# Optimization experiments

Hardware: AMD Instinct MI355X
Metric: run time of the kernel (lower is better)

Reference implementation:

```python
import jax, jax.numpy as jnp
import numpy as np

S, B, H = 256, 64, 1024


def setup_inputs() -> dict:
    key = jax.random.key(0)
    ks = jax.random.split(key, 8)
    scale = 1.0 / np.sqrt(2 * H)  # nn.Linear default-ish scale
    return {
        "x": jax.random.normal(ks[0], (S, B, H), dtype=jnp.float32),
        "h0": jax.random.normal(ks[1], (B, H), dtype=jnp.float32),
        "c0": jax.random.normal(ks[2], (B, H), dtype=jnp.float32),
        "Wf": jax.random.normal(ks[3], (H, 2 * H), dtype=jnp.float32) * scale,
        "bf": jnp.zeros((H,), dtype=jnp.float32),
        "Wi": jax.random.normal(ks[4], (H, 2 * H), dtype=jnp.float32) * scale,
        "bi": jnp.zeros((H,), dtype=jnp.float32),
        "Wg": jax.random.normal(ks[5], (H, 2 * H), dtype=jnp.float32) * scale,
        "bg": jnp.zeros((H,), dtype=jnp.float32),
        "Wo": jax.random.normal(ks[6], (H, 2 * H), dtype=jnp.float32) * scale,
        "bo": jnp.zeros((H,), dtype=jnp.float32),
    }


def _lstm(x, h0, c0, Wf, bf, Wi, bi, Wg, bg, Wo, bo):
    nhid = h0.shape[-1]
    # Fuse the 4 gate Linears into one GEMM: W_all [4H, 2H], b_all [4H].
    W_all = jnp.concatenate([Wf, Wi, Wg, Wo], axis=0)
    b_all = jnp.concatenate([bf, bi, bg, bo], axis=0)
    Wx, Wh = W_all[:, :nhid], W_all[:, nhid:]  # x-part / h-part of cat([x,h])
    # Precompute input contribution for all timesteps: [S, B, 4H]
    xz = jnp.einsum("sbh,gh->sbg", x, Wx) + b_all

    def step(carry, xz_t):
        h, c = carry
        z = xz_t + h @ Wh.T  # [B, 4H]
        f, i, g, o = jnp.split(z, 4, axis=-1)
        f = jax.nn.sigmoid(f)
        i = jax.nn.sigmoid(i)
        g = jnp.tanh(g)
        o = jax.nn.sigmoid(o)
        c = f * c + i * g
        h = o * jnp.tanh(c)
        return (h, c), h

    (h_f, c_f), hseq = jax.lax.scan(step, (h0, c0), xz)
    return hseq, h_f, c_f


def reference(x, h0, c0, Wf, bf, Wi, bi, Wg, bg, Wo, bo):
    hseq, h_f, c_f = _lstm(x, h0, c0, Wf, bf, Wi, bi, Wg, bg, Wo, bo)
    # residual_con=False path in the original: return x + hidden_seq
    return x + hseq, h_f, c_f
```

## Files before the change

kernel.cpp:

```cpp
#include <hip/hip_runtime.h>

typedef __bf16 bf16x8 __attribute__((ext_vector_type(8)));
typedef float f32x4 __attribute__((ext_vector_type(4)));
typedef unsigned int u32x4 __attribute__((ext_vector_type(4)));

#define S_LEN 256
#define BATCH 64
#define HID   1024
#define NWG   256
#define SBH   (S_LEN * BATCH * HID)
#define BH    (BATCH * HID)

__device__ __forceinline__ float sigm(float v) { return 1.0f / (1.0f + __expf(-v)); }
__device__ __forceinline__ float tanh_fast(float v) {
  float e = __expf(-2.0f * __builtin_fabsf(v));
  float r = (1.0f - e) / (1.0f + e);
  return __builtin_copysignf(r, v);
}

__device__ __forceinline__ u32x4 cvt8(float4 a, float4 b) {
  union { unsigned short us[8]; u32x4 v; } r;
  r.us[0] = __builtin_bit_cast(unsigned short, (__bf16)a.x);
  r.us[1] = __builtin_bit_cast(unsigned short, (__bf16)a.y);
  r.us[2] = __builtin_bit_cast(unsigned short, (__bf16)a.z);
  r.us[3] = __builtin_bit_cast(unsigned short, (__bf16)a.w);
  r.us[4] = __builtin_bit_cast(unsigned short, (__bf16)b.x);
  r.us[5] = __builtin_bit_cast(unsigned short, (__bf16)b.y);
  r.us[6] = __builtin_bit_cast(unsigned short, (__bf16)b.z);
  r.us[7] = __builtin_bit_cast(unsigned short, (__bf16)b.w);
  return r.v;
}

#define LOAD8_X4(dst, base, MODS)                                             \
  asm volatile(                                                               \
      "global_load_dwordx4 %0, %8, off offset:0 " MODS "\n\t"                 \
      "global_load_dwordx4 %1, %8, off offset:64 " MODS "\n\t"                \
      "global_load_dwordx4 %2, %8, off offset:128 " MODS "\n\t"               \
      "global_load_dwordx4 %3, %8, off offset:192 " MODS "\n\t"               \
      "global_load_dwordx4 %4, %8, off offset:256 " MODS "\n\t"               \
      "global_load_dwordx4 %5, %8, off offset:320 " MODS "\n\t"               \
      "global_load_dwordx4 %6, %8, off offset:384 " MODS "\n\t"               \
      "global_load_dwordx4 %7, %8, off offset:448 " MODS "\n\t"               \
      "s_waitcnt vmcnt(0)"                                                    \
      : "=&v"((dst)[0]), "=&v"((dst)[1]), "=&v"((dst)[2]), "=&v"((dst)[3]),   \
        "=&v"((dst)[4]), "=&v"((dst)[5]), "=&v"((dst)[6]), "=&v"((dst)[7])    \
      : "v"(base)                                                             \
      : "memory")

__global__ void prep_kernel(const float* __restrict__ x, const float* __restrict__ h0,
                            const float* __restrict__ Wf, const float* __restrict__ Wi,
                            const float* __restrict__ Wg, const float* __restrict__ Wo,
                            __bf16* __restrict__ x_bf, __bf16* __restrict__ w_x,
                            __bf16* __restrict__ w_h, __bf16* __restrict__ h_buf) {
  size_t tid = (size_t)blockIdx.x * blockDim.x + threadIdx.x;
  size_t stride = (size_t)gridDim.x * blockDim.x;

  for (size_t i = tid; i < (size_t)(SBH / 8); i += stride) {
    const float4* s = (const float4*)x + i * 2;
    ((u32x4*)x_bf)[i] = cvt8(s[0], s[1]);
  }

#define W_CONV(W, gidx)                                                        \
  for (size_t i = tid; i < (size_t)(1024 * 128); i += stride) {                \
    int j   = (int)(i >> 7);                                                   \
    int kc8 = (int)(i & 127);                                                  \
    const float* row = (W) + (size_t)j * 2048;                                 \
    const float4* sx = (const float4*)(row + kc8 * 8);                         \
    const float4* sh = (const float4*)(row + 1024 + kc8 * 8);                  \
    size_t dst = (size_t)((gidx) * 1024 + j) * 128 + kc8;                      \
    ((u32x4*)w_x)[dst] = cvt8(sx[0], sx[1]);                                   \
    ((u32x4*)w_h)[dst] = cvt8(sh[0], sh[1]);                                   \
  }
  W_CONV(Wf, 0)
  W_CONV(Wi, 1)
  W_CONV(Wg, 2)
  W_CONV(Wo, 3)
#undef W_CONV

  for (size_t i = tid; i < (size_t)(BH / 8); i += stride) {
    const float4* s = (const float4*)h0 + i * 2;
    u32x4 v = cvt8(s[0], s[1]);
    v &= 0xFFFEFFFEu;
    ((u32x4*)h_buf)[i] = v;
  }

  for (size_t i = tid; i < (size_t)(BH / 8); i += stride) {
    u32x4 p = {0x00010001u, 0x00010001u, 0x00010001u, 0x00010001u};
    ((u32x4*)(h_buf + BH))[i] = p;
  }
}

__global__ __launch_bounds__(256, 1) void lstm_kernel(
    const float* __restrict__ x, const float* __restrict__ c0,
    const float* __restrict__ bfp, const float* __restrict__ bip,
    const float* __restrict__ bgp, const float* __restrict__ bop,
    const __bf16* __restrict__ x_bf, const __bf16* __restrict__ w_x,
    const __bf16* __restrict__ w_h, __bf16* __restrict__ h_buf,
    float* __restrict__ out) {
  const int tid    = threadIdx.x;
  const int wgid   = blockIdx.x;
  const int m_idx  = wgid & 3;
  const int m_base = m_idx * 16;
  const int U      = (wgid >> 2) * 16;
  const int wave   = tid >> 6;
  const int lane   = tid & 63;
  const int l16    = lane & 15;
  const int kq8    = (lane >> 4) * 8;
  const int kbase  = wave * 256;

  __shared__ float zbuf[2][4][16][65];
  __shared__ unsigned short hpack[16][16];

  u32x4 Braw[64];
#pragma unroll
  for (int n = 0; n < 4; ++n) {
    unsigned long gbh =
        (unsigned long)(w_h + (size_t)(n * 1024 + U + l16) * HID + kbase + kq8);
    LOAD8_X4(&Braw[n * 8], gbh, "");
  }
#pragma unroll
  for (int n = 0; n < 4; ++n) {
    unsigned long gbx =
        (unsigned long)(w_x + (size_t)(n * 1024 + U + l16) * HID + kbase + kq8);
    LOAD8_X4(&Braw[32 + n * 8], gbx, "");
  }

  const int b_loc  = tid >> 4;
  const int u_loc  = tid & 15;
  const int j_t    = U + u_loc;
  const int b_glob = m_base + b_loc;
  float c = c0[(size_t)b_glob * HID + j_t];
  const float bias_f = bfp[j_t], bias_i = bip[j_t], bias_g = bgp[j_t], bias_o = bop[j_t];

  u32x4 Araw_x[8];
  {
    const __bf16* xp = x_bf + (size_t)(m_base + l16) * HID + kbase + kq8;
#pragma unroll
    for (int kc = 0; kc < 8; ++kc) Araw_x[kc] = *(const u32x4*)(xp + kc * 32);
  }
  f32x4 accx0 = {0,0,0,0}, accx1 = {0,0,0,0}, accx2 = {0,0,0,0}, accx3 = {0,0,0,0};
#pragma unroll
  for (int kc = 0; kc < 8; ++kc) {
    bf16x8 a = __builtin_bit_cast(bf16x8, Araw_x[kc]);
    accx0 = __builtin_amdgcn_mfma_f32_16x16x32_bf16(a, __builtin_bit_cast(bf16x8, Braw[32 +  0 + kc]), accx0, 0, 0, 0);
    accx1 = __builtin_amdgcn_mfma_f32_16x16x32_bf16(a, __builtin_bit_cast(bf16x8, Braw[32 +  8 + kc]), accx1, 0, 0, 0);
    accx2 = __builtin_amdgcn_mfma_f32_16x16x32_bf16(a, __builtin_bit_cast(bf16x8, Braw[32 + 16 + kc]), accx2, 0, 0, 0);
    accx3 = __builtin_amdgcn_mfma_f32_16x16x32_bf16(a, __builtin_bit_cast(bf16x8, Braw[32 + 24 + kc]), accx3, 0, 0, 0);
  }
  {
    const __bf16* xp = x_bf + (size_t)(BATCH + m_base + l16) * HID + kbase + kq8;
#pragma unroll
    for (int kc = 0; kc < 8; ++kc) Araw_x[kc] = *(const u32x4*)(xp + kc * 32);
  }

  for (int t = 0; t < S_LEN; ++t) {
    const size_t roff = (t & 1) ? (size_t)BH : 0;
    const size_t woff = (t & 1) ? 0 : (size_t)BH;
    const int zp = t & 1;

    u32x4 Araw_h[8];
    {
      unsigned long ga = (unsigned long)(h_buf + roff + (size_t)(m_base + l16) * HID +
                                         kbase + kq8);
      const unsigned mexp = ((unsigned)(t >> 1) & 1u) * 0x00010001u;
      LOAD8_X4(Araw_h, ga, "sc0 sc1");
      while (true) {
        unsigned bad = 0;
#pragma unroll
        for (int kc = 0; kc < 8; ++kc) {
          u32x4 w = Araw_h[kc];
          bad |= ((w[0] ^ mexp) & 0x00010001u);
          bad |= ((w[1] ^ mexp) & 0x00010001u);
          bad |= ((w[2] ^ mexp) & 0x00010001u);
          bad |= ((w[3] ^ mexp) & 0x00010001u);
        }
        if (__ballot(bad != 0) == 0ull) break;
        __builtin_amdgcn_s_sleep(2);
        LOAD8_X4(Araw_h, ga, "sc0 sc1");
      }
    }

    f32x4 acc0 = accx0, acc1 = accx1, acc2 = accx2, acc3 = accx3;
#pragma unroll
    for (int kc = 0; kc < 8; ++kc) {
      bf16x8 a = __builtin_bit_cast(bf16x8, Araw_h[kc]);
      acc0 = __builtin_amdgcn_mfma_f32_16x16x32_bf16(a, __builtin_bit_cast(bf16x8, Braw[ 0 + kc]), acc0, 0, 0, 0);
      acc1 = __builtin_amdgcn_mfma_f32_16x16x32_bf16(a, __builtin_bit_cast(bf16x8, Braw[ 8 + kc]), acc1, 0, 0, 0);
      acc2 = __builtin_amdgcn_mfma_f32_16x16x32_bf16(a, __builtin_bit_cast(bf16x8, Braw[16 + kc]), acc2, 0, 0, 0);
      acc3 = __builtin_amdgcn_mfma_f32_16x16x32_bf16(a, __builtin_bit_cast(bf16x8, Braw[24 + kc]), acc3, 0, 0, 0);
    }

    {
      int q = lane >> 4;
#pragma unroll
      for (int r = 0; r < 4; ++r) {
        zbuf[zp][wave][q * 4 + r][ 0 + l16] = acc0[r];
        zbuf[zp][wave][q * 4 + r][16 + l16] = acc1[r];
        zbuf[zp][wave][q * 4 + r][32 + l16] = acc2[r];
        zbuf[zp][wave][q * 4 + r][48 + l16] = acc3[r];
      }
    }
    __syncthreads();

    float h;
    {
      float zf = 0.f, zi = 0.f, zg = 0.f, zo = 0.f;
#pragma unroll
      for (int w = 0; w < 4; ++w) {
        zf += zbuf[zp][w][b_loc][ 0 + u_loc];
        zi += zbuf[zp][w][b_loc][16 + u_loc];
        zg += zbuf[zp][w][b_loc][32 + u_loc];
        zo += zbuf[zp][w][b_loc][48 + u_loc];
      }
      float fg = sigm(zf + bias_f);
      float ig = sigm(zi + bias_i);
      float gg = tanh_fast(zg + bias_g);
      float og = sigm(zo + bias_o);
      c = fg * c + ig * gg;
      h = og * tanh_fast(c);
    }

    if (t < S_LEN - 1) {
      {
        unsigned short hb = __builtin_bit_cast(unsigned short, (__bf16)h);
        hb = (unsigned short)((hb & 0xFFFEu) | (unsigned)(((t + 1) >> 1) & 1));
        hpack[b_loc][u_loc] = hb;
      }
      asm volatile("s_waitcnt lgkmcnt(0)" ::: "memory");
      __builtin_amdgcn_sched_barrier(0);
      if (lane < 8) {
        int b = 4 * wave + (lane >> 1), half = lane & 1;
        u32x4 hv = *(const u32x4*)(&hpack[b][half * 8]);
        unsigned long ha = (unsigned long)(h_buf + woff +
                                           (size_t)(m_base + b) * HID + U + half * 8);
        asm volatile("global_store_dwordx4 %0, %1, off sc0 sc1"
                     :: "v"(ha), "v"(hv) : "memory");
      }

      {
        size_t oi = ((size_t)(t * BATCH + b_glob)) * HID + j_t;
        out[oi] = x[oi] + h;
      }
      accx0 = (f32x4){0,0,0,0}; accx1 = (f32x4){0,0,0,0};
      accx2 = (f32x4){0,0,0,0}; accx3 = (f32x4){0,0,0,0};
#pragma unroll
      for (int kc = 0; kc < 8; ++kc) {
        bf16x8 a = __builtin_bit_cast(bf16x8, Araw_x[kc]);
        accx0 = __builtin_amdgcn_mfma_f32_16x16x32_bf16(a, __builtin_bit_cast(bf16x8, Braw[32 +  0 + kc]), accx0, 0, 0, 0);
        accx1 = __builtin_amdgcn_mfma_f32_16x16x32_bf16(a, __builtin_bit_cast(bf16x8, Braw[32 +  8 + kc]), accx1, 0, 0, 0);
        accx2 = __builtin_amdgcn_mfma_f32_16x16x32_bf16(a, __builtin_bit_cast(bf16x8, Braw[32 + 16 + kc]), accx2, 0, 0, 0);
        accx3 = __builtin_amdgcn_mfma_f32_16x16x32_bf16(a, __builtin_bit_cast(bf16x8, Braw[32 + 24 + kc]), accx3, 0, 0, 0);
      }
      {
        int tn = (t + 2 < S_LEN) ? (t + 2) : (S_LEN - 1);
        const __bf16* xp =
            x_bf + ((size_t)(tn * BATCH + m_base + l16)) * HID + kbase + kq8;
#pragma unroll
        for (int kc = 0; kc < 8; ++kc) Araw_x[kc] = *(const u32x4*)(xp + kc * 32);
      }
    } else {
      size_t oi = ((size_t)(t * BATCH + b_glob)) * HID + j_t;
      out[oi] = x[oi] + h;
      out[(size_t)SBH + (size_t)b_glob * HID + j_t] = h;
      out[(size_t)SBH + BH + (size_t)b_glob * HID + j_t] = c;
    }
  }
}

extern "C" void kernel_launch(void* const* d_in, const int* in_sizes, int n_in,
                              void* d_out, int out_size, void* d_ws, size_t ws_size,
                              hipStream_t stream) {
  const float* x   = (const float*)d_in[0];
  const float* h0  = (const float*)d_in[1];
  const float* c0  = (const float*)d_in[2];
  const float* Wf  = (const float*)d_in[3];
  const float* bf_ = (const float*)d_in[4];
  const float* Wi  = (const float*)d_in[5];
  const float* bi_ = (const float*)d_in[6];
  const float* Wg  = (const float*)d_in[7];
  const float* bg_ = (const float*)d_in[8];
  const float* Wo  = (const float*)d_in[9];
  const float* bo_ = (const float*)d_in[10];

  char* ws = (char*)d_ws;
  size_t off = 0;
  __bf16* x_bf = (__bf16*)(ws + off); off += (size_t)SBH * 2;
  __bf16* w_x  = (__bf16*)(ws + off); off += (size_t)4 * 1024 * 1024 * 2;
  __bf16* w_h  = (__bf16*)(ws + off); off += (size_t)4 * 1024 * 1024 * 2;
  __bf16* h_buf = (__bf16*)(ws + off); off += (size_t)2 * BH * 2;
  if (ws_size < off) return;

  float* out = (float*)d_out;

  prep_kernel<<<2048, 256, 0, stream>>>(x, h0, Wf, Wi, Wg, Wo, x_bf, w_x, w_h, h_buf);
  lstm_kernel<<<NWG, 256, 0, stream>>>(x, c0, bf_, bi_, bg_, bo_, x_bf, w_x, w_h, h_buf, out);
}
```

Baseline: 1.071 ms.

## Drop x bf16 prepass, issue early h loads, swizzle zbuf LDS

```diff
diff --git a/kernel.cpp b/kernel.cpp
--- a/kernel.cpp
+++ b/kernel.cpp
@@ -47,18 +47,51 @@
       : "v"(base)                                                             \
       : "memory")
 
-__global__ void prep_kernel(const float* __restrict__ x, const float* __restrict__ h0,
+#define CHECK8(H, MEXP, BAD)                                                  \
+  do {                                                                        \
+    BAD = 0;                                                                  \
+    _Pragma("unroll")                                                         \
+    for (int _kc = 0; _kc < 8; ++_kc) {                                       \
+      u32x4 _w = (H)[_kc];                                                    \
+      BAD |= ((_w[0] ^ (MEXP)) & 0x00010001u);                                \
+      BAD |= ((_w[1] ^ (MEXP)) & 0x00010001u);                                \
+      BAD |= ((_w[2] ^ (MEXP)) & 0x00010001u);                                \
+      BAD |= ((_w[3] ^ (MEXP)) & 0x00010001u);                                \
+    }                                                                         \
+  } while (0)
+
+#define HMFMA(H)                                                              \
+  do {                                                                        \
+    _Pragma("unroll")                                                         \
+    for (int _kc = 0; _kc < 8; ++_kc) {                                       \
+      bf16x8 _a = __builtin_bit_cast(bf16x8, (H)[_kc]);                       \
+      acc0 = __builtin_amdgcn_mfma_f32_16x16x32_bf16(_a, __builtin_bit_cast(bf16x8, Braw[ 0 + _kc]), acc0, 0, 0, 0); \
+      acc1 = __builtin_amdgcn_mfma_f32_16x16x32_bf16(_a, __builtin_bit_cast(bf16x8, Braw[ 8 + _kc]), acc1, 0, 0, 0); \
+      acc2 = __builtin_amdgcn_mfma_f32_16x16x32_bf16(_a, __builtin_bit_cast(bf16x8, Braw[16 + _kc]), acc2, 0, 0, 0); \
+      acc3 = __builtin_amdgcn_mfma_f32_16x16x32_bf16(_a, __builtin_bit_cast(bf16x8, Braw[24 + _kc]), acc3, 0, 0, 0); \
+    }                                                                         \
+  } while (0)
+
+#define EARLY_LOAD16(EARR, HB)                                                \
+  do {                                                                        \
+    _Pragma("unroll")                                                         \
+    for (int _kc = 0; _kc < 8; ++_kc) {                                       \
+      (EARR)[2 * _kc] = __hip_atomic_load(                                    \
+          (const unsigned long long*)((HB) + _kc * 32),                       \
+          __ATOMIC_RELAXED, __HIP_MEMORY_SCOPE_AGENT);                        \
+      (EARR)[2 * _kc + 1] = __hip_atomic_load(                                \
+          (const unsigned long long*)((HB) + _kc * 32 + 4),                   \
+          __ATOMIC_RELAXED, __HIP_MEMORY_SCOPE_AGENT);                        \
+    }                                                                         \
+  } while (0)
+
+__global__ void prep_kernel(const float* __restrict__ h0,
                             const float* __restrict__ Wf, const float* __restrict__ Wi,
                             const float* __restrict__ Wg, const float* __restrict__ Wo,
-                            __bf16* __restrict__ x_bf, __bf16* __restrict__ w_x,
-                            __bf16* __restrict__ w_h, __bf16* __restrict__ h_buf) {
+                            __bf16* __restrict__ w_x, __bf16* __restrict__ w_h,
+                            __bf16* __restrict__ h_buf) {
   size_t tid = (size_t)blockIdx.x * blockDim.x + threadIdx.x;
   size_t stride = (size_t)gridDim.x * blockDim.x;
-
-  for (size_t i = tid; i < (size_t)(SBH / 8); i += stride) {
-    const float4* s = (const float4*)x + i * 2;
-    ((u32x4*)x_bf)[i] = cvt8(s[0], s[1]);
-  }
 
 #define W_CONV(W, gidx)                                                        \
   for (size_t i = tid; i < (size_t)(1024 * 128); i += stride) {                \
@@ -94,9 +127,8 @@
     const float* __restrict__ x, const float* __restrict__ c0,
     const float* __restrict__ bfp, const float* __restrict__ bip,
     const float* __restrict__ bgp, const float* __restrict__ bop,
-    const __bf16* __restrict__ x_bf, const __bf16* __restrict__ w_x,
-    const __bf16* __restrict__ w_h, __bf16* __restrict__ h_buf,
-    float* __restrict__ out) {
+    const __bf16* __restrict__ w_x, const __bf16* __restrict__ w_h,
+    __bf16* __restrict__ h_buf, float* __restrict__ out) {
   const int tid    = threadIdx.x;
   const int wgid   = blockIdx.x;
   const int m_idx  = wgid & 3;
@@ -108,7 +140,7 @@
   const int kq8    = (lane >> 4) * 8;
   const int kbase  = wave * 256;
 
-  __shared__ float zbuf[2][4][16][65];
+  __shared__ float zbuf[2][4][16][64];
   __shared__ unsigned short hpack[16][16];
 
   u32x4 Braw[64];
@@ -134,9 +166,13 @@
 
   u32x4 Araw_x[8];
   {
-    const __bf16* xp = x_bf + (size_t)(m_base + l16) * HID + kbase + kq8;
-#pragma unroll
-    for (int kc = 0; kc < 8; ++kc) Araw_x[kc] = *(const u32x4*)(xp + kc * 32);
+    const float* xp = x + (size_t)(m_base + l16) * HID + kbase + kq8;
+#pragma unroll
+    for (int kc = 0; kc < 8; ++kc) {
+      float4 lo = *(const float4*)(xp + kc * 32);
+      float4 hi = *(const float4*)(xp + kc * 32 + 4);
+      Araw_x[kc] = cvt8(lo, hi);
+    }
   }
   f32x4 accx0 = {0,0,0,0}, accx1 = {0,0,0,0}, accx2 = {0,0,0,0}, accx3 = {0,0,0,0};
 #pragma unroll
@@ -148,69 +184,73 @@
     accx3 = __builtin_amdgcn_mfma_f32_16x16x32_bf16(a, __builtin_bit_cast(bf16x8, Braw[32 + 24 + kc]), accx3, 0, 0, 0);
   }
   {
-    const __bf16* xp = x_bf + (size_t)(BATCH + m_base + l16) * HID + kbase + kq8;
-#pragma unroll
-    for (int kc = 0; kc < 8; ++kc) Araw_x[kc] = *(const u32x4*)(xp + kc * 32);
-  }
+    const float* xp = x + ((size_t)BATCH + m_base + l16) * HID + kbase + kq8;
+#pragma unroll
+    for (int kc = 0; kc < 8; ++kc) {
+      float4 lo = *(const float4*)(xp + kc * 32);
+      float4 hi = *(const float4*)(xp + kc * 32 + 4);
+      Araw_x[kc] = cvt8(lo, hi);
+    }
+  }
+
+  const __bf16* hb_base = h_buf + (size_t)(m_base + l16) * HID + kbase + kq8;
+  const unsigned long ga_base = (unsigned long)hb_base;
+
+  unsigned long long e[16];
+  EARLY_LOAD16(e, hb_base);
 
   for (int t = 0; t < S_LEN; ++t) {
     const size_t roff = (t & 1) ? (size_t)BH : 0;
-    const size_t woff = (t & 1) ? 0 : (size_t)BH;
+    const unsigned mexp = ((unsigned)(t >> 1) & 1u) * 0x00010001u;
+    const unsigned long ga = ga_base + roff * 2;
     const int zp = t & 1;
 
-    u32x4 Araw_h[8];
+    f32x4 acc0 = accx0, acc1 = accx1, acc2 = accx2, acc3 = accx3;
     {
-      unsigned long ga = (unsigned long)(h_buf + roff + (size_t)(m_base + l16) * HID +
-                                         kbase + kq8);
-      const unsigned mexp = ((unsigned)(t >> 1) & 1u) * 0x00010001u;
-      LOAD8_X4(Araw_h, ga, "sc0 sc1");
-      while (true) {
-        unsigned bad = 0;
-#pragma unroll
-        for (int kc = 0; kc < 8; ++kc) {
-          u32x4 w = Araw_h[kc];
-          bad |= ((w[0] ^ mexp) & 0x00010001u);
-          bad |= ((w[1] ^ mexp) & 0x00010001u);
-          bad |= ((w[2] ^ mexp) & 0x00010001u);
-          bad |= ((w[3] ^ mexp) & 0x00010001u);
-        }
-        if (__ballot(bad != 0) == 0ull) break;
-        __builtin_amdgcn_s_sleep(2);
-        LOAD8_X4(Araw_h, ga, "sc0 sc1");
-      }
-    }
-
-    f32x4 acc0 = accx0, acc1 = accx1, acc2 = accx2, acc3 = accx3;
-#pragma unroll
-    for (int kc = 0; kc < 8; ++kc) {
-      bf16x8 a = __builtin_bit_cast(bf16x8, Araw_h[kc]);
-      acc0 = __builtin_amdgcn_mfma_f32_16x16x32_bf16(a, __builtin_bit_cast(bf16x8, Braw[ 0 + kc]), acc0, 0, 0, 0);
-      acc1 = __builtin_amdgcn_mfma_f32_16x16x32_bf16(a, __builtin_bit_cast(bf16x8, Braw[ 8 + kc]), acc1, 0, 0, 0);
-      acc2 = __builtin_amdgcn_mfma_f32_16x16x32_bf16(a, __builtin_bit_cast(bf16x8, Braw[16 + kc]), acc2, 0, 0, 0);
-      acc3 = __builtin_amdgcn_mfma_f32_16x16x32_bf16(a, __builtin_bit_cast(bf16x8, Braw[24 + kc]), acc3, 0, 0, 0);
+      u32x4 Ah[8];
+#pragma unroll
+      for (int kc = 0; kc < 8; ++kc) {
+        unsigned long long lo = e[2 * kc], hi = e[2 * kc + 1];
+        Ah[kc] = (u32x4){(unsigned)lo, (unsigned)(lo >> 32),
+                         (unsigned)hi, (unsigned)(hi >> 32)};
+      }
+      unsigned bad;
+      CHECK8(Ah, mexp, bad);
+      if (__builtin_expect(__ballot(bad != 0) != 0ull, 0)) {
+        do {
+          __builtin_amdgcn_s_sleep(1);
+          LOAD8_X4(Ah, ga, "sc0 sc1");
+          CHECK8(Ah, mexp, bad);
+        } while (__ballot(bad != 0) != 0ull);
+      }
+      HMFMA(Ah);
     }
 
     {
       int q = lane >> 4;
 #pragma unroll
       for (int r = 0; r < 4; ++r) {
-        zbuf[zp][wave][q * 4 + r][ 0 + l16] = acc0[r];
-        zbuf[zp][wave][q * 4 + r][16 + l16] = acc1[r];
-        zbuf[zp][wave][q * 4 + r][32 + l16] = acc2[r];
-        zbuf[zp][wave][q * 4 + r][48 + l16] = acc3[r];
+        int row = q * 4 + r;
+        int s = ((row ^ (row >> 2)) & 3) << 4;
+        zbuf[zp][wave][row][( 0 + l16) ^ s] = acc0[r];
+        zbuf[zp][wave][row][(16 + l16) ^ s] = acc1[r];
+        zbuf[zp][wave][row][(32 + l16) ^ s] = acc2[r];
+        zbuf[zp][wave][row][(48 + l16) ^ s] = acc3[r];
       }
     }
     __syncthreads();
 
     float h;
     {
+      const int row = b_loc;
+      const int s = ((row ^ (row >> 2)) & 3) << 4;
       float zf = 0.f, zi = 0.f, zg = 0.f, zo = 0.f;
 #pragma unroll
       for (int w = 0; w < 4; ++w) {
-        zf += zbuf[zp][w][b_loc][ 0 + u_loc];
-        zi += zbuf[zp][w][b_loc][16 + u_loc];
-        zg += zbuf[zp][w][b_loc][32 + u_loc];
-        zo += zbuf[zp][w][b_loc][48 + u_loc];
+        zf += zbuf[zp][w][row][( 0 + u_loc) ^ s];
+        zi += zbuf[zp][w][row][(16 + u_loc) ^ s];
+        zg += zbuf[zp][w][row][(32 + u_loc) ^ s];
+        zo += zbuf[zp][w][row][(48 + u_loc) ^ s];
       }
       float fg = sigm(zf + bias_f);
       float ig = sigm(zi + bias_i);
@@ -221,10 +261,12 @@
     }
 
     if (t < S_LEN - 1) {
+      const size_t woff = (t & 1) ? 0 : (size_t)BH;
+
       {
-        unsigned short hb = __builtin_bit_cast(unsigned short, (__bf16)h);
-        hb = (unsigned short)((hb & 0xFFFEu) | (unsigned)(((t + 1) >> 1) & 1));
-        hpack[b_loc][u_loc] = hb;
+        unsigned short hbv = __builtin_bit_cast(unsigned short, (__bf16)h);
+        hbv = (unsigned short)((hbv & 0xFFFEu) | (unsigned)(((t + 1) >> 1) & 1));
+        hpack[b_loc][u_loc] = hbv;
       }
       asm volatile("s_waitcnt lgkmcnt(0)" ::: "memory");
       __builtin_amdgcn_sched_barrier(0);
@@ -237,6 +279,8 @@
                      :: "v"(ha), "v"(hv) : "memory");
       }
 
+      EARLY_LOAD16(e, hb_base + woff);
+
       {
         size_t oi = ((size_t)(t * BATCH + b_glob)) * HID + j_t;
         out[oi] = x[oi] + h;
@@ -253,10 +297,13 @@
       }
       {
         int tn = (t + 2 < S_LEN) ? (t + 2) : (S_LEN - 1);
-        const __bf16* xp =
-            x_bf + ((size_t)(tn * BATCH + m_base + l16)) * HID + kbase + kq8;
-#pragma unroll
-        for (int kc = 0; kc < 8; ++kc) Araw_x[kc] = *(const u32x4*)(xp + kc * 32);
+        const float* xp = x + ((size_t)(tn * BATCH + m_base + l16)) * HID + kbase + kq8;
+#pragma unroll
+        for (int kc = 0; kc < 8; ++kc) {
+          float4 lo = *(const float4*)(xp + kc * 32);
+          float4 hi = *(const float4*)(xp + kc * 32 + 4);
+          Araw_x[kc] = cvt8(lo, hi);
+        }
       }
     } else {
       size_t oi = ((size_t)(t * BATCH + b_glob)) * HID + j_t;
@@ -284,7 +331,6 @@
 
   char* ws = (char*)d_ws;
   size_t off = 0;
-  __bf16* x_bf = (__bf16*)(ws + off); off += (size_t)SBH * 2;
   __bf16* w_x  = (__bf16*)(ws + off); off += (size_t)4 * 1024 * 1024 * 2;
   __bf16* w_h  = (__bf16*)(ws + off); off += (size_t)4 * 1024 * 1024 * 2;
   __bf16* h_buf = (__bf16*)(ws + off); off += (size_t)2 * BH * 2;
@@ -292,6 +338,6 @@
 
   float* out = (float*)d_out;
 
-  prep_kernel<<<2048, 256, 0, stream>>>(x, h0, Wf, Wi, Wg, Wo, x_bf, w_x, w_h, h_buf);
-  lstm_kernel<<<NWG, 256, 0, stream>>>(x, c0, bf_, bi_, bg_, bo_, x_bf, w_x, w_h, h_buf, out);
-}
+  prep_kernel<<<2048, 256, 0, stream>>>(h0, Wf, Wi, Wg, Wo, w_x, w_h, h_buf);
+  lstm_kernel<<<NWG, 256, 0, stream>>>(x, c0, bf_, bi_, bg_, bo_, w_x, w_h, h_buf, out);
+}
```

Result: slower. 3.013 ms (+181.4%).
